# Performance work log

Measured on AMD Instinct MI355X. Metric: run time of the kernel, lower is better.

## Reference

```python
import jax, jax.numpy as jnp
import numpy as np

B, L, H = 2, 2048, 2048
NH, D = 16, 128          # num_heads, head_dim
MLP = 4 * H              # mlp_hidden_dim = int(hidden_size * mlp_ratio)


def setup_inputs() -> dict:
    key = jax.random.key(0)
    ks = jax.random.split(key, 8)
    x = jax.random.normal(ks[0], (B, L, H), jnp.float32)
    vec = jax.random.normal(ks[1], (B, H), jnp.float32)
    pe = jax.random.normal(ks[2], (B, 1, L, D // 2, 2, 2), jnp.float32)
    # Modulation(dim, is_double=False): Linear(H, 3H)
    mod_w = 0.02 * jax.random.normal(ks[3], (3 * H, H), jnp.float32)
    mod_b = jnp.zeros((3 * H,), jnp.float32)
    # linear1: Linear(H, 3H + MLP)
    lin1_w = 0.02 * jax.random.normal(ks[4], (3 * H + MLP, H), jnp.float32)
    lin1_b = jnp.zeros((3 * H + MLP,), jnp.float32)
    # linear2: Linear(H + MLP, H)
    lin2_w = 0.02 * jax.random.normal(ks[5], (H, H + MLP), jnp.float32)
    lin2_b = jnp.zeros((H,), jnp.float32)
    # QKNorm: RMSNorm scales over head_dim
    q_scale = jnp.ones((D,), jnp.float32)
    k_scale = jnp.ones((D,), jnp.float32)
    return dict(x=x, vec=vec, pe=pe, mod_w=mod_w, mod_b=mod_b,
                lin1_w=lin1_w, lin1_b=lin1_b, lin2_w=lin2_w, lin2_b=lin2_b,
                q_scale=q_scale, k_scale=k_scale)


def _layernorm(x, eps=1e-6):
    mu = jnp.mean(x, axis=-1, keepdims=True)
    var = jnp.mean((x - mu) ** 2, axis=-1, keepdims=True)
    return (x - mu) * jax.lax.rsqrt(var + eps)


def _rmsnorm(x, scale, eps=1e-6):
    return x * jax.lax.rsqrt(jnp.mean(x * x, axis=-1, keepdims=True) + eps) * scale


def _apply_rope(t, pe):
    # t: [B, NH, L, D]; pe: [B, 1, L, D//2, 2, 2]
    t_ = t.reshape(*t.shape[:-1], D // 2, 1, 2)
    out = pe[..., 0] * t_[..., 0] + pe[..., 1] * t_[..., 1]  # [B, NH, L, D//2, 2]
    return out.reshape(*t.shape)


def reference(x, vec, pe, mod_w, mod_b, lin1_w, lin1_b, lin2_w, lin2_b, q_scale, k_scale):
    # Modulation: silu -> linear -> (shift, scale, gate), each [B, 1, H]
    mod = jax.nn.silu(vec) @ mod_w.T + mod_b
    shift, scale, gate = jnp.split(mod[:, None, :], 3, axis=-1)

    x_mod = (1.0 + scale) * _layernorm(x) + shift

    h = x_mod @ lin1_w.T + lin1_b            # [B, L, 3H + MLP]
    qkv, mlp = h[..., :3 * H], h[..., 3 * H:]

    # 'B L (K H D) -> K B H L D'
    qkv = qkv.reshape(B, L, 3, NH, D).transpose(2, 0, 3, 1, 4)
    q, k, v = qkv[0], qkv[1], qkv[2]

    q = _rmsnorm(q, q_scale)
    k = _rmsnorm(k, k_scale)

    q = _apply_rope(q, pe)
    k = _apply_rope(k, pe)

    # SDPA with default scale 1/sqrt(D)
    logits = jnp.einsum('bhqd,bhkd->bhqk', q, k) / jnp.sqrt(jnp.float32(D))
    probs = jax.nn.softmax(logits, axis=-1)
    attn = jnp.einsum('bhqk,bhkd->bhqd', probs, v)          # [B, NH, L, D]
    attn = attn.transpose(0, 2, 1, 3).reshape(B, L, H)      # 'B H L D -> B L (H D)'

    mlp_act = jax.nn.gelu(mlp, approximate=True)
    out = jnp.concatenate([attn, mlp_act], axis=-1) @ lin2_w.T + lin2_b
    return x + gate * out
```

## Files before the change

### kernel.cpp

```cpp
#include <hip/hip_runtime.h>

#define LSEQ 2048
#define HDIM 2048
#define NHEAD 16
#define DHEAD 128
#define N1 14336
#define NC 10240

typedef unsigned short u16;
typedef __attribute__((ext_vector_type(8))) short short8;
typedef __attribute__((ext_vector_type(4))) float f32x4;

#define ASYNC16(g, l) __builtin_amdgcn_global_load_lds( \
    (__attribute__((address_space(1))) void*)(g),        \
    (__attribute__((address_space(3))) void*)(l), 16, 0, 0)

__device__ __forceinline__ u16 f2bf(float f) {
  unsigned u = __builtin_bit_cast(unsigned, f);
  u += 0x7fffu + ((u >> 16) & 1u);
  return (u16)(u >> 16);
}
__device__ __forceinline__ u16 f2bf_trunc(float f) {
  return (u16)(__builtin_bit_cast(unsigned, f) >> 16);
}
__device__ __forceinline__ float bf2f(u16 v) {
  unsigned u = ((unsigned)v) << 16;
  return __builtin_bit_cast(float, u);
}
__device__ __forceinline__ float silu_f(float x) { return x / (1.f + __expf(-x)); }
__device__ __forceinline__ float gelu_f(float x) {
  float u = 0.7978845608028654f * (x + 0.044715f * x * x * x);
  float e = __expf(2.f * u);
  float th = 1.f - 2.f / (e + 1.f);
  return 0.5f * x * (1.f + th);
}

__global__ __launch_bounds__(256) void k_mod(const float* __restrict__ vec,
                                             const float* __restrict__ mod_w,
                                             const float* __restrict__ mod_b,
                                             float* __restrict__ modv) {
  int j = blockIdx.x, t = threadIdx.x;
  const float4* wr = (const float4*)(mod_w + (size_t)j * HDIM);
  const float4* vv = (const float4*)vec;
  float s0 = 0.f, s1 = 0.f;
#pragma unroll
  for (int i = 0; i < 2; i++) {
    int idx = t + i * 256;
    float4 w = wr[idx];
    float4 a = vv[idx];
    float4 c = vv[idx + 512];
    s0 += w.x*silu_f(a.x) + w.y*silu_f(a.y) + w.z*silu_f(a.z) + w.w*silu_f(a.w);
    s1 += w.x*silu_f(c.x) + w.y*silu_f(c.y) + w.z*silu_f(c.z) + w.w*silu_f(c.w);
  }
  int lane = t & 63, wid = t >> 6;
#pragma unroll
  for (int o = 32; o; o >>= 1) { s0 += __shfl_down(s0, o, 64); s1 += __shfl_down(s1, o, 64); }
  __shared__ float red[8];
  if (!lane) { red[wid] = s0; red[4 + wid] = s1; }
  __syncthreads();
  if (!t) {
    float b_ = mod_b[j];
    modv[j] = red[0]+red[1]+red[2]+red[3] + b_;
    modv[3*HDIM + j] = red[4]+red[5]+red[6]+red[7] + b_;
  }
}

__global__ __launch_bounds__(256) void k_ln(const float* __restrict__ x,
                                            const float* __restrict__ modv,
                                            u16* __restrict__ xmod) {
  int row = blockIdx.x, t = threadIdx.x;
  int b = row >> 11;
  const float4* xr = (const float4*)(x + (size_t)row * HDIM);
  float4 v0 = xr[t], v1 = xr[t + 256];
  float sum = v0.x+v0.y+v0.z+v0.w + v1.x+v1.y+v1.z+v1.w;
  float sq  = v0.x*v0.x+v0.y*v0.y+v0.z*v0.z+v0.w*v0.w
            + v1.x*v1.x+v1.y*v1.y+v1.z*v1.z+v1.w*v1.w;
  int lane = t & 63, wid = t >> 6;
#pragma unroll
  for (int o = 32; o; o >>= 1) { sum += __shfl_down(sum, o, 64); sq += __shfl_down(sq, o, 64); }
  __shared__ float red[8];
  if (!lane) { red[wid] = sum; red[4+wid] = sq; }
  __syncthreads();
  sum = red[0]+red[1]+red[2]+red[3];
  sq  = red[4]+red[5]+red[6]+red[7];
  float mu = sum * (1.f/HDIM);
  float rstd = rsqrtf(sq * (1.f/HDIM) - mu*mu + 1e-6f);
  const float* mb = modv + b * (3*HDIM);
  u16* orow = xmod + (size_t)row * HDIM;
  float vv[8] = {v0.x,v0.y,v0.z,v0.w,v1.x,v1.y,v1.z,v1.w};
#pragma unroll
  for (int half = 0; half < 2; half++) {
    int h0 = (t + half*256) * 4;
    ushort4 o4;
    float e0 = (1.f + mb[HDIM + h0+0]) * ((vv[half*4+0]-mu)*rstd) + mb[h0+0];
    float e1 = (1.f + mb[HDIM + h0+1]) * ((vv[half*4+1]-mu)*rstd) + mb[h0+1];
    float e2 = (1.f + mb[HDIM + h0+2]) * ((vv[half*4+2]-mu)*rstd) + mb[h0+2];
    float e3 = (1.f + mb[HDIM + h0+3]) * ((vv[half*4+3]-mu)*rstd) + mb[h0+3];
    o4.x = f2bf(e0); o4.y = f2bf(e1); o4.z = f2bf(e2); o4.w = f2bf(e3);
    *(ushort4*)(orow + h0) = o4;
  }
}

__global__ __launch_bounds__(256) void k_cvt(const float4* __restrict__ src,
                                             ushort4* __restrict__ dst, int n4) {
  int i = blockIdx.x * 256 + threadIdx.x;
  int stride = gridDim.x * 256;
  for (; i < n4; i += stride) {
    float4 v = src[i];
    ushort4 o;
    o.x = f2bf(v.x); o.y = f2bf(v.y); o.z = f2bf(v.z); o.w = f2bf(v.w);
    dst[i] = o;
  }
}

__global__ __launch_bounds__(256, 2) void k_gemm1(const u16* __restrict__ A,
                                                  const u16* __restrict__ Bw,
                                                  const float* __restrict__ bias,
                                                  u16* __restrict__ qkv,
                                                  u16* __restrict__ cat) {
  const int K = HDIM;
  int bid = blockIdx.x;
  int bm = bid & 31, bn = bid >> 5;
  int t = threadIdx.x, wave = t >> 6, lane = t & 63;
  int wm = wave >> 1, wn = wave & 1;
  __shared__ u16 S[128 * 136];
  u16* As0 = S;
  u16* As1 = S + 4096;
  u16* Bs0 = S + 8192;
  u16* Bs1 = S + 12288;
  const f32x4 fzero = {0.f, 0.f, 0.f, 0.f};
  f32x4 acc[4][4];
#pragma unroll
  for (int i = 0; i < 4; i++)
#pragma unroll
    for (int j2 = 0; j2 < 4; j2++) acc[i][j2] = fzero;
  const u16* Ab = A + (size_t)bm * 128 * K;
  const u16* Bb = Bw + (size_t)bn * 128 * K;
  int r4 = lane >> 2, c4 = lane & 3;
  int fm = lane & 15, fk = (lane >> 4) * 8, fq = lane >> 4;
  for (int k0 = 0; k0 < K; k0 += 64) {
#pragma unroll
    for (int i = 0; i < 2; i++) {
      int row = wave*32 + i*16;
      const u16* ar = Ab + (size_t)(row + r4)*K + k0 + c4*8;
      const u16* br = Bb + (size_t)(row + r4)*K + k0 + c4*8;
      ASYNC16(ar,      &As0[row*32]);
      ASYNC16(ar + 32, &As1[row*32]);
      ASYNC16(br,      &Bs0[row*32]);
      ASYNC16(br + 32, &Bs1[row*32]);
    }
    __syncthreads();
#pragma unroll
    for (int p = 0; p < 2; p++) {
      const u16* Ap = p ? As1 : As0;
      const u16* Bp = p ? Bs1 : Bs0;
      short8 af[4], bfr[4];
#pragma unroll
      for (int mt = 0; mt < 4; mt++)
        af[mt] = *(const short8*)&Ap[(wm*64 + mt*16 + fm)*32 + fk];
#pragma unroll
      for (int nt = 0; nt < 4; nt++)
        bfr[nt] = *(const short8*)&Bp[(wn*64 + nt*16 + fm)*32 + fk];
#pragma unroll
      for (int mt = 0; mt < 4; mt++)
#pragma unroll
        for (int nt = 0; nt < 4; nt++)
          acc[mt][nt] = __builtin_amdgcn_mfma_f32_16x16x32_bf16(af[mt], bfr[nt], acc[mt][nt], 0, 0, 0);
    }
    __syncthreads();
  }
  bool ismlp = (bn >= 48);
#pragma unroll
  for (int nt = 0; nt < 4; nt++) {
    int col_l = wn*64 + nt*16 + fm;
    float bv = bias[bn*128 + col_l];
#pragma unroll
    for (int mt = 0; mt < 4; mt++) {
#pragma unroll
      for (int rr = 0; rr < 4; rr++) {
        int row_l = wm*64 + mt*16 + fq*4 + rr;
        float v = acc[mt][nt][rr] + bv;
        if (ismlp) v = gelu_f(v);
        S[row_l*136 + col_l] = f2bf(v);
      }
    }
  }
  __syncthreads();
  int c = (t & 15) * 8;
  int rq = t >> 4;
#pragma unroll
  for (int p = 0; p < 8; p++) {
    int r_l = p*16 + rq;
    short8 v = *(const short8*)&S[r_l*136 + c];
    int row_g = bm*128 + r_l;
    if (!ismlp)
      *(short8*)(qkv + (size_t)row_g*(3*HDIM) + bn*128 + c) = v;
    else
      *(short8*)(cat + (size_t)row_g*NC + HDIM + (bn-48)*128 + c) = v;
  }
}

__global__ __launch_bounds__(256, 2) void k_gemm2(const u16* __restrict__ A,
                                                  const u16* __restrict__ Bw,
                                                  const float* __restrict__ bias,
                                                  const float* __restrict__ xres,
                                                  const float* __restrict__ modv,
                                                  float* __restrict__ out) {
  const int K = NC;
  int bid = blockIdx.x;
  int bm = bid & 31, bn = bid >> 5;
  int t = threadIdx.x, wave = t >> 6, lane = t & 63;
  int wm = wave >> 1, wn = wave & 1;
  __shared__ u16 As[2*128*32];
  __shared__ u16 Bs[2*128*32];
  const f32x4 fzero = {0.f, 0.f, 0.f, 0.f};
  f32x4 acc[4][4];
#pragma unroll
  for (int i = 0; i < 4; i++)
#pragma unroll
    for (int j2 = 0; j2 < 4; j2++) acc[i][j2] = fzero;
  const u16* Ab = A + (size_t)bm * 128 * K;
  const u16* Bb = Bw + (size_t)bn * 128 * K;
  int r4 = lane >> 2, c4 = lane & 3;
  int fm = lane & 15, fk = (lane >> 4) * 8;
  for (int k0 = 0; k0 < K; k0 += 64) {
#pragma unroll
    for (int i = 0; i < 2; i++) {
      int row = wave*32 + i*16;
      const u16* ar = Ab + (size_t)(row + r4)*K + k0 + c4*8;
      const u16* br = Bb + (size_t)(row + r4)*K + k0 + c4*8;
      ASYNC16(ar,      &As[row*32]);
      ASYNC16(ar + 32, &As[4096 + row*32]);
      ASYNC16(br,      &Bs[row*32]);
      ASYNC16(br + 32, &Bs[4096 + row*32]);
    }
    __syncthreads();
#pragma unroll
    for (int p = 0; p < 2; p++) {
      const u16* Ap = &As[p*4096];
      const u16* Bp = &Bs[p*4096];
      short8 af[4], bfr[4];
#pragma unroll
      for (int mt = 0; mt < 4; mt++)
        af[mt] = *(const short8*)&Ap[(wm*64 + mt*16 + fm)*32 + fk];
#pragma unroll
      for (int nt = 0; nt < 4; nt++)
        bfr[nt] = *(const short8*)&Bp[(wn*64 + nt*16 + fm)*32 + fk];
#pragma unroll
      for (int mt = 0; mt < 4; mt++)
#pragma unroll
        for (int nt = 0; nt < 4; nt++)
          acc[mt][nt] = __builtin_amdgcn_mfma_f32_16x16x32_bf16(af[mt], bfr[nt], acc[mt][nt], 0, 0, 0);
    }
    __syncthreads();
  }
  int rbase = bm*128 + wm*64;
  int cbase = bn*128 + wn*64;
  int b = (bm*128) >> 11;
#pragma unroll
  for (int nt = 0; nt < 4; nt++) {
    int col = cbase + nt*16 + fm;
    float bv = bias[col];
    float g = modv[b*(3*HDIM) + 2*HDIM + col];
#pragma unroll
    for (int mt = 0; mt < 4; mt++) {
#pragma unroll
      for (int rr = 0; rr < 4; rr++) {
        int row = rbase + mt*16 + (lane>>4)*4 + rr;
        size_t idx = (size_t)row*HDIM + col;
        out[idx] = xres[idx] + g * (acc[mt][nt][rr] + bv);
      }
    }
  }
}

__global__ __launch_bounds__(256) void k_qk(const u16* __restrict__ qkv,
                                            const float* __restrict__ pe,
                                            const float* __restrict__ q_scale,
                                            const float* __restrict__ k_scale,
                                            u16* __restrict__ Q, u16* __restrict__ Ko) {
  int bid = blockIdx.x;
  int l = bid & (LSEQ-1);
  int b = bid >> 11;
  int t = threadIdx.x;
  int h = t >> 4;
  int dc = (t & 15) * 8;
  const u16* base = qkv + (size_t)bid * (3*HDIM);
  short8 q8 = *(const short8*)(base + h*DHEAD + dc);
  short8 k8 = *(const short8*)(base + HDIM + h*DHEAD + dc);
  float qf[8], kf[8];
  float sq = 0.f, sk = 0.f;
#pragma unroll
  for (int i = 0; i < 8; i++) {
    qf[i] = bf2f((u16)q8[i]); kf[i] = bf2f((u16)k8[i]);
    sq += qf[i]*qf[i]; sk += kf[i]*kf[i];
  }
#pragma unroll
  for (int m = 1; m < 16; m <<= 1) { sq += __shfl_xor(sq, m, 64); sk += __shfl_xor(sk, m, 64); }
  float rq = rsqrtf(sq * (1.f/DHEAD) + 1e-6f);
  float rk = rsqrtf(sk * (1.f/DHEAD) + 1e-6f);
  float4 qs0 = *(const float4*)(q_scale + dc), qs1 = *(const float4*)(q_scale + dc + 4);
  float4 ks0 = *(const float4*)(k_scale + dc), ks1 = *(const float4*)(k_scale + dc + 4);
  float qsc[8] = {qs0.x,qs0.y,qs0.z,qs0.w,qs1.x,qs1.y,qs1.z,qs1.w};
  float ksc[8] = {ks0.x,ks0.y,ks0.z,ks0.w,ks1.x,ks1.y,ks1.z,ks1.w};
  float qn[8], kn[8];
#pragma unroll
  for (int i = 0; i < 8; i++) { qn[i] = qf[i]*rq*qsc[i]; kn[i] = kf[i]*rk*ksc[i]; }
  const float4* pe4 = (const float4*)pe + ((size_t)bid*64 + (dc >> 1));
  short8 qo, ko;
#pragma unroll
  for (int pi = 0; pi < 4; pi++) {
    float4 pp = pe4[pi];
    float q0 = pp.x*qn[2*pi] + pp.y*qn[2*pi+1];
    float q1 = pp.z*qn[2*pi] + pp.w*qn[2*pi+1];
    float k0 = pp.x*kn[2*pi] + pp.y*kn[2*pi+1];
    float k1 = pp.z*kn[2*pi] + pp.w*kn[2*pi+1];
    qo[2*pi] = (short)f2bf(q0); qo[2*pi+1] = (short)f2bf(q1);
    ko[2*pi] = (short)f2bf(k0); ko[2*pi+1] = (short)f2bf(k1);
  }
  size_t oidx = (((size_t)(b*NHEAD + h))*LSEQ + l)*DHEAD + dc;
  *(short8*)(Q + oidx) = qo;
  *(short8*)(Ko + oidx) = ko;
}

__global__ __launch_bounds__(256) void k_vt(const u16* __restrict__ qkv, u16* __restrict__ Vt) {
  int bid = blockIdx.x;
  int lt = bid & 31, h = (bid >> 5) & 15, b = bid >> 9;
  __shared__ u16 tile[64][132];
  int t = threadIdx.x;
#pragma unroll
  for (int it = 0; it < 8; it++) {
    int idx = it*1024 + t*4;
    int li = idx >> 7, di = idx & 127;
    const u16* src = qkv + ((size_t)(b*LSEQ + lt*64 + li))*(3*HDIM) + 2*HDIM + h*DHEAD + di;
    ushort4 v = *(const ushort4*)src;
    *(ushort4*)&tile[li][di] = v;
  }
  __syncthreads();
  u16* dst = Vt + ((size_t)(b*NHEAD + h))*DHEAD*LSEQ + lt*64;
#pragma unroll
  for (int it = 0; it < 32; it++) {
    int idx = it*256 + t;
    int lo = idx & 63, dd = idx >> 6;
    dst[(size_t)dd*LSEQ + lo] = tile[lo][dd];
  }
}

#define SC2 0.12753329583f
__global__ __launch_bounds__(256, 2) void k_attn(const u16* __restrict__ Q,
                                                 const u16* __restrict__ Kc,
                                                 const u16* __restrict__ Vt,
                                                 u16* __restrict__ cat) {
  __shared__ u16 Ks[2*64*128];
  __shared__ u16 Vs[2*128*64];
  __shared__ u16 Ps[64*88];
  int bid = blockIdx.x;
  int bh = bid & 31, qt = bid >> 5;
  int h = bh & 15, b = bh >> 4;
  int t = threadIdx.x, wave = t >> 6, lane = t & 63;
  int fm = lane & 15, fq = lane >> 4;
  int r8 = lane >> 3, c8 = lane & 7;
  const u16* Qg = Q  + (((size_t)(b*NHEAD + h))*LSEQ + qt*64) * DHEAD;
  const u16* Kg = Kc + ((size_t)(b*NHEAD + h))*LSEQ * DHEAD;
  const u16* Vg = Vt + ((size_t)(b*NHEAD + h))*DHEAD*LSEQ;
  short8 aq[4];
#pragma unroll
  for (int ks = 0; ks < 4; ks++)
    aq[ks] = *(const short8*)(Qg + (size_t)(wave*16 + fm)*DHEAD + ks*32 + fq*8);
#pragma unroll
  for (int i = 0; i < 4; i++) {
    int row = wave*16 + i*4;
    ASYNC16(Kg + (size_t)(row + fq)*DHEAD + fm*8, &Ks[row*DHEAD]);
    int vrow = wave*32 + i*8;
    ASYNC16(Vg + (size_t)(vrow + r8)*LSEQ + c8*8, &Vs[vrow*64]);
  }
  const f32x4 fzero = {0.f, 0.f, 0.f, 0.f};
  f32x4 o[8];
#pragma unroll
  for (int i = 0; i < 8; i++) o[i] = fzero;
  float lsum[4] = {0.f, 0.f, 0.f, 0.f};
  for (int kt = 0; kt < 32; kt++) {
    int cur = kt & 1;
    __syncthreads();
    if (kt < 31) {
      int off = (cur ^ 1) * 8192;
      const u16* Kt_ = Kg + (size_t)(kt+1)*64*DHEAD;
      const u16* Vt_ = Vg + (kt+1)*64;
#pragma unroll
      for (int i = 0; i < 4; i++) {
        int row = wave*16 + i*4;
        ASYNC16(Kt_ + (size_t)(row + fq)*DHEAD + fm*8, &Ks[off + row*DHEAD]);
        int vrow = wave*32 + i*8;
        ASYNC16(Vt_ + (size_t)(vrow + r8)*LSEQ + c8*8, &Vs[off + vrow*64]);
      }
    }
    const u16* Kb = &Ks[cur*8192];
    const u16* Vb = &Vs[cur*8192];
    f32x4 s[4];
#pragma unroll
    for (int nt = 0; nt < 4; nt++) s[nt] = fzero;
#pragma unroll
    for (int ks = 0; ks < 4; ks++) {
#pragma unroll
      for (int nt = 0; nt < 4; nt++) {
        short8 bk = *(const short8*)&Kb[(nt*16 + fm)*DHEAD + ks*32 + fq*8];
        s[nt] = __builtin_amdgcn_mfma_f32_16x16x32_bf16(aq[ks], bk, s[nt], 0, 0, 0);
      }
    }
#pragma unroll
    for (int nt = 0; nt < 4; nt++)
#pragma unroll
      for (int r = 0; r < 4; r++) {
        float p = exp2f(s[nt][r] * SC2);
        s[nt][r] = p;
        lsum[r] += p;
      }
#pragma unroll
    for (int nt = 0; nt < 4; nt++)
#pragma unroll
      for (int r = 0; r < 4; r++)
        Ps[(wave*16 + fq*4 + r)*88 + nt*16 + fm] = f2bf_trunc(s[nt][r]);
    asm volatile("s_waitcnt lgkmcnt(0)" ::: "memory");
#pragma unroll
    for (int ks2 = 0; ks2 < 2; ks2++) {
      short8 ap = *(const short8*)&Ps[(wave*16 + fm)*88 + ks2*32 + fq*8];
#pragma unroll
      for (int nt = 0; nt < 8; nt++) {
        short8 bv = *(const short8*)&Vb[(nt*16 + fm)*64 + ks2*32 + fq*8];
        o[nt] = __builtin_amdgcn_mfma_f32_16x16x32_bf16(ap, bv, o[nt], 0, 0, 0);
      }
    }
  }
#pragma unroll
  for (int r = 0; r < 4; r++) {
#pragma unroll
    for (int o2 = 8; o2 >= 1; o2 >>= 1) lsum[r] += __shfl_xor(lsum[r], o2, 64);
  }
#pragma unroll
  for (int nt = 0; nt < 8; nt++) {
#pragma unroll
    for (int r = 0; r < 4; r++) {
      int l = qt*64 + wave*16 + fq*4 + r;
      int d = nt*16 + fm;
      float v = o[nt][r] / lsum[r];
      cat[((size_t)(b*LSEQ + l))*NC + h*DHEAD + d] = f2bf(v);
    }
  }
}

extern "C" void kernel_launch(void* const* d_in, const int* in_sizes, int n_in,
                              void* d_out, int out_size, void* d_ws, size_t ws_size,
                              hipStream_t stream) {
  const float* x       = (const float*)d_in[0];
  const float* vec     = (const float*)d_in[1];
  const float* pe      = (const float*)d_in[2];
  const float* mod_w   = (const float*)d_in[3];
  const float* mod_b   = (const float*)d_in[4];
  const float* lin1_w  = (const float*)d_in[5];
  const float* lin1_b  = (const float*)d_in[6];
  const float* lin2_w  = (const float*)d_in[7];
  const float* lin2_b  = (const float*)d_in[8];
  const float* q_scale = (const float*)d_in[9];
  const float* k_scale = (const float*)d_in[10];
  char* ws = (char*)d_ws;

  float* modv = (float*)(ws + 0);
  u16* xmod  = (u16*)(ws + 65536ULL);
  u16* qkv   = (u16*)(ws + 16842752ULL);
  u16* w2    = (u16*)(ws + 16842752ULL);
  u16* cat   = (u16*)(ws + 67174400ULL);
  u16* w1    = (u16*)(ws + 151060480ULL);
  u16* Qb    = (u16*)(ws + 151060480ULL);
  u16* Kb    = (u16*)(ws + 167837696ULL);
  u16* Vtb   = (u16*)(ws + 184614912ULL);

  k_mod<<<dim3(3*HDIM), dim3(256), 0, stream>>>(vec, mod_w, mod_b, modv);
  k_cvt<<<dim3(4096), dim3(256), 0, stream>>>((const float4*)lin1_w, (ushort4*)w1, (N1*HDIM)/4);
  k_ln<<<dim3(4096), dim3(256), 0, stream>>>(x, modv, xmod);
  k_gemm1<<<dim3(32*112), dim3(256), 0, stream>>>(xmod, w1, lin1_b, qkv, cat);
  k_qk<<<dim3(4096), dim3(256), 0, stream>>>(qkv, pe, q_scale, k_scale, Qb, Kb);
  k_vt<<<dim3(1024), dim3(256), 0, stream>>>(qkv, Vtb);
  k_cvt<<<dim3(4096), dim3(256), 0, stream>>>((const float4*)lin2_w, (ushort4*)w2, (HDIM*NC)/4);
  k_attn<<<dim3(1024), dim3(256), 0, stream>>>(Qb, Kb, Vtb, cat);
  k_gemm2<<<dim3(32*16), dim3(256), 0, stream>>>(cat, w2, lin2_b, x, modv, (float*)d_out);
}
```

Measured before the change: 996.1 us.

## Rewrite gemm1 as 256x256 tiled, double-buffered, swizzled 8-wave pipelined kernel

The first GEMM moves from 128x128 tiles with 4 waves and a single-stage load/sync loop to 256x256 tiles with 8 waves. It double-buffers K=64 slices in 128KB of LDS, uses an XOR swizzle to avoid bank conflicts, and interleaves async global-to-LDS loads with MFMA quadrants using vmcnt waits and setprio. Block IDs are remapped so the tiles sharing a column stripe run together, which should improve L2 reuse. The larger tile raises arithmetic intensity and hides memory latency, but 128KB of LDS per block with launch_bounds(512,2) may limit occupancy, and the epilogue becomes two serial halves.

After: 1.034 ms. +3.8%, slower.

```diff
diff --git a/kernel.cpp b/kernel.cpp
--- a/kernel.cpp
+++ b/kernel.cpp
@@ -113,90 +113,151 @@
   }
 }
 
-__global__ __launch_bounds__(256, 2) void k_gemm1(const u16* __restrict__ A,
+#define FENCE asm volatile("" ::: "memory")
+#define BARRIER { FENCE; __builtin_amdgcn_s_barrier(); FENCE; }
+#define WAITVM(n) asm volatile("s_waitcnt vmcnt(" #n ")" ::: "memory")
+
+#define ABUF(bufv) (S + (bufv)*16384)
+#define BBUF(bufv) (S + 32768 + (bufv)*16384)
+
+#define STG_A(bufv, rbase, kk) do { \
+    int r_ = (rbase) + wave * 8; \
+    ASYNC16(Ab + (size_t)(r_ + lr) * K + (kk) + sg * 8, ABUF(bufv) + r_ * 64); \
+  } while (0)
+#define STG_B(bufv, rbase, kk) do { \
+    int r_ = (rbase) + (wave >> 2) * 64 + (wave & 3) * 8; \
+    ASYNC16(Bb + (size_t)(r_ + lr) * K + (kk) + sg * 8, BBUF(bufv) + r_ * 64); \
+  } while (0)
+#define STG_U0(bufv, kk) { STG_A(bufv, 0, kk);   STG_A(bufv, 128, kk); }
+#define STG_U1(bufv, kk) { STG_A(bufv, 64, kk);  STG_A(bufv, 192, kk); }
+#define STG_U2(bufv, kk) { STG_B(bufv, 0, kk);   STG_B(bufv, 128, kk); }
+#define STG_U3(bufv, kk) { STG_B(bufv, 32, kk);  STG_B(bufv, 160, kk); }
+
+#define LDS_A(qmv, bufv) do { \
+    const u16* p_ = ABUF(bufv); \
+    _Pragma("unroll") for (int mt = 0; mt < 4; mt++) { \
+      int row_ = wm*128 + (qmv)*64 + mt*16 + fm; \
+      _Pragma("unroll") for (int ks = 0; ks < 2; ks++) \
+        a[mt][ks] = *(const short8*)(p_ + row_*64 + (((ks*4 + fq) ^ (fm & 7)) * 8)); \
+    } } while (0)
+#define LDS_Bv(dst, qnv, bufv) do { \
+    const u16* p_ = BBUF(bufv); \
+    _Pragma("unroll") for (int nt = 0; nt < 2; nt++) { \
+      int row_ = wn*64 + (qnv)*32 + nt*16 + fm; \
+      _Pragma("unroll") for (int ks = 0; ks < 2; ks++) \
+        dst[nt][ks] = *(const short8*)(p_ + row_*64 + (((ks*4 + fq) ^ (fm & 7)) * 8)); \
+    } } while (0)
+
+#define MMQ(qmv, qnv, bsel) do { \
+    __builtin_amdgcn_s_setprio(1); \
+    _Pragma("unroll") for (int mt = 0; mt < 4; mt++) \
+    _Pragma("unroll") for (int nt = 0; nt < 2; nt++) \
+    _Pragma("unroll") for (int ks = 0; ks < 2; ks++) \
+      acc[(qmv)*4 + mt][(qnv)*2 + nt] = __builtin_amdgcn_mfma_f32_16x16x32_bf16( \
+          a[mt][ks], bsel[nt][ks], acc[(qmv)*4 + mt][(qnv)*2 + nt], 0, 0, 0); \
+    __builtin_amdgcn_s_setprio(0); } while (0)
+
+#define PHASE_Q00(bufv, STAGE, VMN) { LDS_A(0, bufv); LDS_Bv(b0, 0, bufv); STAGE; BARRIER; \
+                                      MMQ(0, 0, b0); WAITVM(VMN); BARRIER; }
+#define PHASE_Q01(bufv, STAGE, VMN) { LDS_Bv(b1, 1, bufv); STAGE; BARRIER; \
+                                      MMQ(0, 1, b1); WAITVM(VMN); BARRIER; }
+#define PHASE_Q11(bufv, STAGE, VMN) { LDS_A(1, bufv); STAGE; BARRIER; \
+                                      MMQ(1, 1, b1); WAITVM(VMN); BARRIER; }
+#define PHASE_Q10(bufv, STAGE, VMN) { STAGE; BARRIER; \
+                                      MMQ(1, 0, b0); WAITVM(VMN); BARRIER; }
+
+__global__ __launch_bounds__(512, 2) void k_gemm1(const u16* __restrict__ A,
                                                   const u16* __restrict__ Bw,
                                                   const float* __restrict__ bias,
                                                   u16* __restrict__ qkv,
                                                   u16* __restrict__ cat) {
   const int K = HDIM;
-  int bid = blockIdx.x;
-  int bm = bid & 31, bn = bid >> 5;
+  const int NT = K / 64;
+  int orig = blockIdx.x;
+  int bid = (orig & 7) * 112 + (orig >> 3);
+  int bm = bid & 15, bn = bid >> 4;
   int t = threadIdx.x, wave = t >> 6, lane = t & 63;
-  int wm = wave >> 1, wn = wave & 1;
-  __shared__ u16 S[128 * 136];
-  u16* As0 = S;
-  u16* As1 = S + 4096;
-  u16* Bs0 = S + 8192;
-  u16* Bs1 = S + 12288;
+  int wm = wave >> 2, wn = wave & 3;
+  int fm = lane & 15, fq = lane >> 4;
+  int lr = lane >> 3, lg = lane & 7;
+  int sg = lg ^ lr;
+
+  __shared__ u16 S[65536];
+
+  const u16* Ab = A + (size_t)bm * 256 * K;
+  const u16* Bb = Bw + (size_t)bn * 256 * K;
+
   const f32x4 fzero = {0.f, 0.f, 0.f, 0.f};
-  f32x4 acc[4][4];
-#pragma unroll
-  for (int i = 0; i < 4; i++)
+  f32x4 acc[8][4];
+#pragma unroll
+  for (int i = 0; i < 8; i++)
 #pragma unroll
     for (int j2 = 0; j2 < 4; j2++) acc[i][j2] = fzero;
-  const u16* Ab = A + (size_t)bm * 128 * K;
-  const u16* Bb = Bw + (size_t)bn * 128 * K;
-  int r4 = lane >> 2, c4 = lane & 3;
-  int fm = lane & 15, fk = (lane >> 4) * 8, fq = lane >> 4;
-  for (int k0 = 0; k0 < K; k0 += 64) {
-#pragma unroll
-    for (int i = 0; i < 2; i++) {
-      int row = wave*32 + i*16;
-      const u16* ar = Ab + (size_t)(row + r4)*K + k0 + c4*8;
-      const u16* br = Bb + (size_t)(row + r4)*K + k0 + c4*8;
-      ASYNC16(ar,      &As0[row*32]);
-      ASYNC16(ar + 32, &As1[row*32]);
-      ASYNC16(br,      &Bs0[row*32]);
-      ASYNC16(br + 32, &Bs1[row*32]);
-    }
-    __syncthreads();
-#pragma unroll
-    for (int p = 0; p < 2; p++) {
-      const u16* Ap = p ? As1 : As0;
-      const u16* Bp = p ? Bs1 : Bs0;
-      short8 af[4], bfr[4];
-#pragma unroll
-      for (int mt = 0; mt < 4; mt++)
-        af[mt] = *(const short8*)&Ap[(wm*64 + mt*16 + fm)*32 + fk];
-#pragma unroll
-      for (int nt = 0; nt < 4; nt++)
-        bfr[nt] = *(const short8*)&Bp[(wn*64 + nt*16 + fm)*32 + fk];
-#pragma unroll
-      for (int mt = 0; mt < 4; mt++)
-#pragma unroll
-        for (int nt = 0; nt < 4; nt++)
-          acc[mt][nt] = __builtin_amdgcn_mfma_f32_16x16x32_bf16(af[mt], bfr[nt], acc[mt][nt], 0, 0, 0);
-    }
-    __syncthreads();
-  }
-  bool ismlp = (bn >= 48);
-#pragma unroll
-  for (int nt = 0; nt < 4; nt++) {
-    int col_l = wn*64 + nt*16 + fm;
-    float bv = bias[bn*128 + col_l];
-#pragma unroll
-    for (int mt = 0; mt < 4; mt++) {
-#pragma unroll
-      for (int rr = 0; rr < 4; rr++) {
-        int row_l = wm*64 + mt*16 + fq*4 + rr;
-        float v = acc[mt][nt][rr] + bv;
-        if (ismlp) v = gelu_f(v);
-        S[row_l*136 + col_l] = f2bf(v);
+  short8 a[4][2], b0[2][2], b1[2][2];
+
+  STG_U0(0, 0); STG_U2(0, 0); STG_U3(0, 0); STG_U1(0, 0);
+  WAITVM(4); BARRIER;
+
+  const int NIT = NT / 2;
+  for (int it2 = 0; it2 < NIT - 1; ++it2) {
+    int kB = it2 * 128 + 64;
+    int kC = it2 * 128 + 128;
+    PHASE_Q00(0, STG_U0(1, kB), 4);
+    PHASE_Q01(0, STG_U2(1, kB), 4);
+    PHASE_Q11(0, STG_U3(1, kB), 4);
+    PHASE_Q10(0, STG_U1(1, kB), 4);
+    PHASE_Q00(1, STG_U0(0, kC), 4);
+    PHASE_Q01(1, STG_U2(0, kC), 4);
+    PHASE_Q11(1, STG_U3(0, kC), 4);
+    PHASE_Q10(1, STG_U1(0, kC), 4);
+  }
+  {
+    int kB = (NT - 1) * 64;
+    PHASE_Q00(0, STG_U0(1, kB), 4);
+    PHASE_Q01(0, STG_U2(1, kB), 4);
+    PHASE_Q11(0, STG_U3(1, kB), 4);
+    PHASE_Q10(0, STG_U1(1, kB), 4);
+    PHASE_Q00(1, ((void)0), 2);
+    PHASE_Q01(1, ((void)0), 0);
+    PHASE_Q11(1, ((void)0), 0);
+    PHASE_Q10(1, ((void)0), 0);
+  }
+
+  bool ismlp = (bn >= 24);
+  const int EP = 264;
+  u16* Sep = S;
+#pragma unroll
+  for (int half = 0; half < 2; half++) {
+    BARRIER;
+    if (wm == half) {
+#pragma unroll
+      for (int j = 0; j < 4; j++) {
+        int col_l = wn*64 + j*16 + fm;
+        float bv = bias[bn*256 + col_l];
+#pragma unroll
+        for (int i = 0; i < 8; i++) {
+#pragma unroll
+          for (int rr = 0; rr < 4; rr++) {
+            float v = acc[i][j][rr] + bv;
+            if (ismlp) v = gelu_f(v);
+            Sep[(i*16 + fq*4 + rr)*EP + col_l] = f2bf(v);
+          }
+        }
       }
     }
-  }
-  __syncthreads();
-  int c = (t & 15) * 8;
-  int rq = t >> 4;
-#pragma unroll
-  for (int p = 0; p < 8; p++) {
-    int r_l = p*16 + rq;
-    short8 v = *(const short8*)&S[r_l*136 + c];
-    int row_g = bm*128 + r_l;
-    if (!ismlp)
-      *(short8*)(qkv + (size_t)row_g*(3*HDIM) + bn*128 + c) = v;
-    else
-      *(short8*)(cat + (size_t)row_g*NC + HDIM + (bn-48)*128 + c) = v;
+    BARRIER;
+    int cg = (t & 31) * 8;
+    int r0 = t >> 5;
+#pragma unroll
+    for (int p = 0; p < 8; p++) {
+      int r_l = p*16 + r0;
+      short8 v = *(const short8*)&Sep[r_l*EP + cg];
+      int row_g = bm*256 + half*128 + r_l;
+      if (!ismlp)
+        *(short8*)(qkv + (size_t)row_g*(3*HDIM) + bn*256 + cg) = v;
+      else
+        *(short8*)(cat + (size_t)row_g*NC + HDIM + (bn-24)*256 + cg) = v;
+    }
   }
 }
 
@@ -477,7 +538,7 @@
   k_mod<<<dim3(3*HDIM), dim3(256), 0, stream>>>(vec, mod_w, mod_b, modv);
   k_cvt<<<dim3(4096), dim3(256), 0, stream>>>((const float4*)lin1_w, (ushort4*)w1, (N1*HDIM)/4);
   k_ln<<<dim3(4096), dim3(256), 0, stream>>>(x, modv, xmod);
-  k_gemm1<<<dim3(32*112), dim3(256), 0, stream>>>(xmod, w1, lin1_b, qkv, cat);
+  k_gemm1<<<dim3(896), dim3(512), 0, stream>>>(xmod, w1, lin1_b, qkv, cat);
   k_qk<<<dim3(4096), dim3(256), 0, stream>>>(qkv, pe, q_scale, k_scale, Qb, Kb);
   k_vt<<<dim3(1024), dim3(256), 0, stream>>>(qkv, Vtb);
   k_cvt<<<dim3(4096), dim3(256), 0, stream>>>((const float4*)lin2_w, (ushort4*)w2, (HDIM*NC)/4);
```
